# Performance work log

Hardware: AMD Instinct MI355X
Metric: run time of the kernel (lower is better)

The kernel has to match this reference:

```python
import jax, jax.numpy as jnp
import numpy as np

# dims: N batch, I input ch, R recurrent ch, A attention ch, HEADS, O out ch, HxW spatial
N, I, R, A, HEADS, O, H, W = 8, 128, 256, 256, 8, 256, 36, 36
HC = A // HEADS  # head channels


def _conv(x, w, pad):
    # NCHW conv, stride 1
    return jax.lax.conv_general_dilated(x, w, (1, 1), pad,
                                        dimension_numbers=('NCHW', 'OIHW', 'NCHW'))


def setup_inputs() -> dict:
    key = jax.random.key(0)
    ks = jax.random.split(key, 16)

    def wgt(k, shape):
        fan_in = int(np.prod(shape[1:]))
        return jax.random.normal(k, shape, jnp.float32) * (1.0 / float(np.sqrt(fan_in)))

    # gate biases: [init_input=-1 | init_forget=1 | 0 | 0] per CvtLstm init
    b_g = jnp.concatenate([jnp.full((R,), -1.0), jnp.full((R,), 1.0),
                           jnp.zeros((R,)), jnp.zeros((R,))]).astype(jnp.float32)

    return {
        'x': jax.random.normal(ks[0], (N, I, H, W), jnp.float32),
        'w_in': wgt(ks[1], (R, I, 1, 1)), 'b_in': jnp.zeros((R,), jnp.float32),
        'w_qx': wgt(ks[2], (A, R, 3, 3)), 'w_qh': wgt(ks[3], (A, R, 3, 3)),
        'w_kx': wgt(ks[4], (A, R, 3, 3)), 'w_kh': wgt(ks[5], (A, R, 3, 3)),
        'w_vx': wgt(ks[6], (A, R, 3, 3)), 'w_vh': wgt(ks[7], (A, R, 3, 3)),
        'w_ga': wgt(ks[8], (4 * R, A, 1, 1)), 'b_g': b_g,
        'w_gx': wgt(ks[9], (4 * R, R, 1, 1)), 'w_gh': wgt(ks[10], (4 * R, R, 1, 1)),
        'w_out': wgt(ks[11], (O, R, 1, 1)), 'b_out': jnp.zeros((O,), jnp.float32),
    }


def reference(x, w_in, b_in, w_qx, w_qh, w_kx, w_kh, w_vx, w_vh,
              w_ga, b_g, w_gx, w_gh, w_out, b_out):
    # input accumulate: 1x1 conv + bias
    xin = _conv(x, w_in, 'SAME') + b_in[None, :, None, None]
    # first step: recurrent state is zeros (past is empty)
    h = jnp.zeros_like(xin)
    c = jnp.zeros_like(xin)
    # Q: 3x3 padded conv on x and h (accumulated); K/V: 3x3 unpadded -> smaller token set
    q = (_conv(xin, w_qx, 'SAME') + _conv(h, w_qh, 'SAME')).reshape(N, HEADS, HC, H * W)
    k4 = _conv(xin, w_kx, 'VALID') + _conv(h, w_kh, 'VALID')   # [N, A, H-2, W-2]
    D = k4.shape[2] * k4.shape[3]
    k = k4.reshape(N, HEADS, HC, D)
    v = (_conv(xin, w_vx, 'VALID') + _conv(h, w_vh, 'VALID')).reshape(N, HEADS, HC, D)
    # attention: softmax over K/V tokens (dim D)
    attn = jax.nn.softmax(jnp.einsum('nhcq,nhcd->nhqd', q, k), axis=3)  # [N,HEADS,Q,D]
    a = jnp.einsum('nhcd,nhqd->nhcq', v, attn).reshape(N, A, H, W)
    # fused i/f/g/o gate projections: 1x1 conv on a + bias + 1x1 skips on x and h
    gates = (_conv(a, w_ga, 'SAME') + b_g[None, :, None, None]
             + _conv(xin, w_gx, 'SAME') + _conv(h, w_gh, 'SAME'))
    gi, gf, gg, go = jnp.split(gates, 4, axis=1)
    c = jax.nn.sigmoid(gf) * c + jax.nn.sigmoid(gi) * jnp.tanh(gg)
    hn = jax.nn.sigmoid(go) * jnp.tanh(c)
    # output 1x1 conv (dropout p=0 -> identity)
    return _conv(hn, w_out, 'SAME') + b_out[None, :, None, None]
```

## Files before the change

### kernel.cpp

```cpp
#include <hip/hip_runtime.h>
#include <math.h>

typedef unsigned int u32;
typedef unsigned short u16;
typedef unsigned long long u64;
typedef __attribute__((ext_vector_type(8))) __bf16 bf8;
typedef __attribute__((ext_vector_type(4))) float f4;

#define MFMA(a,b,c) __builtin_amdgcn_mfma_f32_16x16x32_bf16(a,b,c,0,0,0)

#define SWC(row_, c_) ((((((c_)>>1) ^ (((row_)>>3)&1))<<1) | (((c_)&1) ^ (((row_)>>4)&1))))

static __device__ __forceinline__ u32 cvtpk(float lo, float hi) {
  u32 r; asm("v_cvt_pk_bf16_f32 %0, %1, %2" : "=v"(r) : "v"(lo), "v"(hi));
  return r;
}
static __device__ __forceinline__ u16 f2b(float x) { return (u16)cvtpk(x, 0.f); }
static __device__ __forceinline__ float sigm(float x) { return 1.f/(1.f+__expf(-x)); }


__global__ __launch_bounds__(256) void k_prep(const float* __restrict__ w_in,
        const float* __restrict__ w_out,
        const float* __restrict__ wqx, const float* __restrict__ wkx,
        const float* __restrict__ wvx,
        const float* __restrict__ w_ga, const float* __restrict__ w_gx,
        u16* __restrict__ winb, u16* __restrict__ woutb,
        u16* __restrict__ tq, u16* __restrict__ tk, u16* __restrict__ tv,
        u16* __restrict__ wg) {
  int task = blockIdx.y;
  int i = blockIdx.x*256 + threadIdx.x;
  if (task == 0) {
    if (i < 32768) winb[i] = f2b(w_in[i]);
    else if (i < 98304) woutb[i - 32768] = f2b(w_out[i - 32768]);
  } else if (task <= 3) {
    if (i < 589824) {
      const float* w = (task==1)?wqx:(task==2)?wkx:wvx;
      u16* wt = (task==1)?tq:(task==2)?tk:tv;
      int e = i & 7, li = (i>>3) & 15, gr = (i>>7) & 3, mb = (i>>9) & 15, it = i >> 13;
      int tap = it >> 3, kg = it & 7;
      int m = mb*16 + li, k = kg*32 + gr*8 + e;
      wt[i] = f2b(w[(size_t)m*2304 + k*9 + tap]);
    }
  } else {
    if (i < 393216) {
      int g = i >> 17, rem = i & 131071, rr = rem >> 9, kk = rem & 511;
      int gb = (g == 0) ? 0 : (g == 1) ? 512 : 768;
      float v = (kk < 256) ? w_ga[(size_t)(gb+rr)*256 + kk]
                           : w_gx[(size_t)(gb+rr)*256 + kk - 256];
      wg[i] = f2b(v);
    }
  }
}

__global__ __launch_bounds__(256,2) void k_xin(const float* __restrict__ x,
        const u16* __restrict__ wb, const float* __restrict__ bias,
        u16* __restrict__ out) {
  __shared__ alignas(16) u16 Xs[128][40];
  __shared__ alignas(16) u16 Ws[128][40];
  int tid = threadIdx.x, lane = tid & 63, wid = tid >> 6;
  int li = lane & 15, gr = lane >> 4;
  int p0 = blockIdx.x*128, m0 = blockIdx.y*128, n = blockIdx.z;
  int pcol = tid & 127, rg = tid >> 7;
  int wrow = tid >> 1, wh = tid & 1;
  int p = p0 + pcol;
  const float* src = x + (size_t)n*128*1296;
  const u32* wb32 = (const u32*)wb;
  f4 z = {0.f,0.f,0.f,0.f};
  f4 acc[4][4];
  #pragma unroll
  for (int i=0;i<4;i++) { acc[i][0]=z; acc[i][1]=z; acc[i][2]=z; acc[i][3]=z; }
  int wm = (wid & 1)*64, wp = (wid >> 1)*64;
  for (int k0 = 0; k0 < 128; k0 += 32) {
    u32 rx[8];
    #pragma unroll
    for (int j = 0; j < 8; j++) {
      int rp = rg*8 + j;
      float a = 0.f, b = 0.f;
      if (p < 1296) { a = src[(size_t)(k0+2*rp)*1296+p]; b = src[(size_t)(k0+2*rp+1)*1296+p]; }
      rx[j] = cvtpk(a, b);
    }
    const u32* wsrc = wb32 + (size_t)(m0+wrow)*64 + (k0>>1) + wh*8;
    int4 rwA = *(const int4*)wsrc, rwB = *(const int4*)(wsrc+4);
    *(int4*)&Xs[pcol][SWC(pcol,2*rg)*8]   = *(int4*)&rx[0];
    *(int4*)&Xs[pcol][SWC(pcol,2*rg+1)*8] = *(int4*)&rx[4];
    *(int4*)&Ws[wrow][SWC(wrow,2*wh)*8]   = rwA;
    *(int4*)&Ws[wrow][SWC(wrow,2*wh+1)*8] = rwB;
    __syncthreads();
    bf8 af[4], bx[4];
    #pragma unroll
    for (int mt=0;mt<4;mt++) { int r = wm+mt*16+li; af[mt] = *(bf8*)&Ws[r][SWC(r,gr)*8]; }
    #pragma unroll
    for (int pt=0;pt<4;pt++) { int r = wp+pt*16+li; bx[pt] = *(bf8*)&Xs[r][SWC(r,gr)*8]; }
    #pragma unroll
    for (int mt=0;mt<4;mt++)
      #pragma unroll
      for (int pt=0;pt<4;pt++)
        acc[mt][pt] = MFMA(af[mt], bx[pt], acc[mt][pt]);
    __syncthreads();
  }
  u32* out32 = (u32*)out + (size_t)n*128*1296;
  #pragma unroll
  for (int mt=0;mt<4;mt++)
    #pragma unroll
    for (int pt=0;pt<4;pt++) {
      int mb = m0 + wm + mt*16 + gr*4;
      int pp = p0 + wp + pt*16 + li;
      if (pp < 1296) {
        out32[(size_t)(mb>>1)*1296 + pp] = cvtpk(acc[mt][pt][0]+bias[mb], acc[mt][pt][1]+bias[mb+1]);
        out32[(size_t)((mb>>1)+1)*1296 + pp] = cvtpk(acc[mt][pt][2]+bias[mb+2], acc[mt][pt][3]+bias[mb+3]);
      }
    }
}

__global__ __launch_bounds__(256,2) void k_conv3(const u16* __restrict__ xin,
        const u16* __restrict__ wq, const u16* __restrict__ wk, const u16* __restrict__ wv,
        u16* __restrict__ qb, u16* __restrict__ kb, u16* __restrict__ vb) {
  __shared__ alignas(16) u16 Xs[2][256][32];
  int tid = threadIdx.x, lane = tid & 63, wid = tid >> 6;
  int li = lane & 15, gr = lane >> 4;
  int tile = blockIdx.x, m0 = blockIdx.y*64, n = blockIdx.z;
  int kind, t0;
  if (tile < 6)       { kind = 0; t0 = tile; }
  else if (tile < 11) { kind = 1; t0 = tile - 6; }
  else                { kind = 2; t0 = tile - 11; }
  int P  = kind ? 1156 : 1296;
  int WO = kind ? 34 : 36;
  int pad = kind ? 0 : 1;
  int px0 = t0*256;
  const u16* wt = (kind==0) ? wq : (kind==1) ? wk : wv;
  const u32* src32 = (const u32*)xin + (size_t)n*128*1296;
  const int4* wt4 = (const int4*)wt;
  int p = px0 + tid;
  bool pvld = p < P;
  int py = 0, px = 0;
  if (pvld) { py = p / WO; px = p % WO; }
  int fx = (tid >> 1) & 3;
  int fr = (li >> 1) & 3;
  int mb0 = m0 >> 4;
  f4 z = {0.f,0.f,0.f,0.f};
  f4 acc[4][4];
  #pragma unroll
  for (int i=0;i<4;i++) { acc[i][0]=z; acc[i][1]=z; acc[i][2]=z; acc[i][3]=z; }
  u32 xA[16], xB[16];
  int4 wA[4], wB[4];

  #define LOADX(it_, X) { \
    int tap_ = (it_) >> 3, kg_ = (it_) & 7; \
    int sy = py + tap_/3 - pad, sx = px + tap_%3 - pad; \
    bool ok = pvld && sy >= 0 && sy < 36 && sx >= 0 && sx < 36; \
    const u32* xs = src32 + (size_t)(kg_*16)*1296 + sy*36 + sx; \
    _Pragma("unroll") \
    for (int j = 0; j < 16; j++) X[j] = ok ? xs[(size_t)j*1296] : 0u; }

  #define LOADW(it_, W) { \
    const int4* wsrc = wt4 + ((size_t)(it_)*16 + mb0)*64 + lane; \
    _Pragma("unroll") \
    for (int mt = 0; mt < 4; mt++) W[mt] = wsrc[(size_t)mt*64]; }

  #define WRITEX(X, b_) { \
    _Pragma("unroll") \
    for (int c = 0; c < 4; c++) \
      *(int4*)&Xs[b_][tid][(c ^ fx)*8] = *(int4*)&X[c*4]; }

  #define MFMAIT(b_, W) { \
    bf8 bx[4]; \
    _Pragma("unroll") \
    for (int pt=0;pt<4;pt++) { \
      int r = wid*64 + pt*16 + li; \
      bx[pt] = *(bf8*)&Xs[b_][r][(gr ^ fr)*8]; \
    } \
    _Pragma("unroll") \
    for (int mt=0;mt<4;mt++) \
      _Pragma("unroll") \
      for (int pt=0;pt<4;pt++) \
        acc[mt][pt] = MFMA(*(bf8*)&W[mt], bx[pt], acc[mt][pt]); }

  LOADX(0, xA); LOADW(0, wA);
  WRITEX(xA, 0);
  LOADX(1, xB); LOADW(1, wB);
  for (int h = 0; h < 35; h++) {
    MFMAIT(0, wA);
    WRITEX(xB, 1);
    LOADX(2*h+2, xA); LOADW(2*h+2, wA);
    MFMAIT(1, wB);
    WRITEX(xA, 0);
    LOADX(2*h+3, xB); LOADW(2*h+3, wB);
  }
  MFMAIT(0, wA);
  WRITEX(xB, 1);
  MFMAIT(1, wB);
  #undef LOADX
  #undef LOADW
  #undef WRITEX
  #undef MFMAIT

  if (kind <= 1) {
    u32* dst32 = (u32*)(kind==0 ? qb : kb) + (size_t)n*128*P;
    #pragma unroll
    for (int mt=0;mt<4;mt++)
      #pragma unroll
      for (int pt=0;pt<4;pt++) {
        int mb = m0 + mt*16 + gr*4;
        int pp = px0 + wid*64 + pt*16 + li;
        if (pp < P) {
          dst32[(size_t)(mb>>1)*P + pp] = cvtpk(acc[mt][pt][0], acc[mt][pt][1]);
          dst32[(size_t)((mb>>1)+1)*P + pp] = cvtpk(acc[mt][pt][2], acc[mt][pt][3]);
        }
      }
  } else {
    #pragma unroll
    for (int mt=0;mt<4;mt++)
      #pragma unroll
      for (int pt=0;pt<4;pt++) {
        int pp = px0 + wid*64 + pt*16 + li;
        if (pp < P) {
          #pragma unroll
          for (int j=0;j<4;j++) {
            int m = m0 + mt*16 + gr*4 + j;
            vb[((size_t)n*256 + m)*1156 + pp] = f2b(acc[mt][pt][j]);
          }
        }
      }
  }
}

__global__ __launch_bounds__(256,2) void k_attn(const u16* __restrict__ qbf,
        const u16* __restrict__ kbf, const u16* __restrict__ vbf, u16* __restrict__ abf) {
  __shared__ alignas(16) u16 Qs[128][40];
  __shared__ alignas(16) u16 Ks[64][40];
  __shared__ alignas(16) u16 Vs[2][32][40];
  __shared__ alignas(16) u16 Ps[4][2][32][40];
  int tid = threadIdx.x, lane = tid & 63, wid = tid >> 6;
  int li = lane & 15, gr = lane >> 4;
  int h = blockIdx.y, n = blockIdx.z;
  int q0 = blockIdx.x*128;
  const u32* Qp32 = (const u32*)qbf + ((size_t)n*128 + h*16)*1296;
  const u32* Kp32 = (const u32*)kbf + ((size_t)n*128 + h*16)*1156;
  const u16* Vp = vbf + ((size_t)n*256 + h*32)*1156;
  #pragma unroll
  for (int j = 0; j < 8; j++) {
    int idx = tid + j*256, qq = idx >> 4, cp = idx & 15;
    int gq = q0 + qq;
    ((u32*)&Qs[qq][0])[cp] = (gq < 1296) ? Qp32[(size_t)cp*1296 + gq] : 0u;
  }
  f4 z = {0.f,0.f,0.f,0.f};
  float mx[2] = {-1e30f, -1e30f}, ls[2] = {0.f, 0.f};
  f4 accO[2][2] = {{z,z},{z,z}};
  int wq = wid*32;
  int kdd = tid >> 2, kq = tid & 3;
  __syncthreads();
  for (int d0 = 0; d0 < 1156; d0 += 64) {
    {
      u32 kk[4];
      int gd = d0 + kdd;
      #pragma unroll
      for (int i = 0; i < 4; i++)
        kk[i] = (gd < 1156) ? Kp32[(size_t)(kq*4+i)*1156 + gd] : 0u;
      *(int4*)&Ks[kdd][SWC(kdd,kq)*8] = *(int4*)&kk[0];
    }
    #pragma unroll
    for (int j = 0; j < 4; j++) {
      int idx = tid + j*256, half = idx >> 9, rem = idx & 511;
      int cc = rem >> 4, dp = rem & 15;
      int gd = d0 + half*32 + dp*2; u32 v = 0;
      if (gd < 1156) v = *(const u32*)&Vp[(size_t)cc*1156 + gd];
      ((u32*)&Vs[half][cc][0])[dp] = v;
    }
    __syncthreads();
    bf8 ak[4], bq[2];
    #pragma unroll
    for (int dt=0;dt<4;dt++) { int r = dt*16+li; ak[dt] = *(bf8*)&Ks[r][SWC(r,gr)*8]; }
    #pragma unroll
    for (int qt=0;qt<2;qt++) bq[qt] = *(bf8*)&Qs[wq + qt*16 + li][8*gr];
    f4 s[2][4];
    #pragma unroll
    for (int qt=0;qt<2;qt++)
      #pragma unroll
      for (int dt=0;dt<4;dt++)
        s[qt][dt] = MFMA(ak[dt], bq[qt], z);
    bool tail = (d0 + 64 > 1156);
    #pragma unroll
    for (int qt=0;qt<2;qt++) {
      if (tail) {
        #pragma unroll
        for (int dt=0;dt<4;dt++)
          #pragma unroll
          for (int j=0;j<4;j++)
            if (d0 + dt*16 + gr*4 + j >= 1156) s[qt][dt][j] = -1e30f;
      }
      float tm = -1e30f;
      #pragma unroll
      for (int dt=0;dt<4;dt++)
        #pragma unroll
        for (int j=0;j<4;j++) tm = fmaxf(tm, s[qt][dt][j]);
      tm = fmaxf(tm, __shfl_xor(tm, 16));
      tm = fmaxf(tm, __shfl_xor(tm, 32));
      if (__any(tm > mx[qt] + 8.f)) {
        float nm = fmaxf(mx[qt], tm);
        float corr = __expf(mx[qt] - nm);
        mx[qt] = nm;
        ls[qt] *= corr;
        accO[0][qt] *= corr; accO[1][qt] *= corr;
      }
      float rs = 0.f;
      #pragma unroll
      for (int dt=0;dt<4;dt++)
        #pragma unroll
        for (int j=0;j<4;j++) {
          float e = __expf(s[qt][dt][j] - mx[qt]);
          s[qt][dt][j] = e; rs += e;
        }
      rs += __shfl_xor(rs, 16); rs += __shfl_xor(rs, 32);
      ls[qt] += rs;
      #pragma unroll
      for (int dt=0;dt<4;dt++) {
        u32 lo_ = cvtpk(s[qt][dt][0], s[qt][dt][1]);
        u32 hi_ = cvtpk(s[qt][dt][2], s[qt][dt][3]);
        u64 pk = (u64)lo_ | ((u64)hi_ << 32);
        *(u64*)&Ps[wid][dt>>1][qt*16 + li][(dt&1)*16 + gr*4] = pk;
      }
    }
    #pragma unroll
    for (int kt=0;kt<2;kt++) {
      bf8 av0 = *(bf8*)&Vs[kt][li][8*gr];
      bf8 av1 = *(bf8*)&Vs[kt][16 + li][8*gr];
      bf8 bp0 = *(bf8*)&Ps[wid][kt][li][8*gr];
      bf8 bp1 = *(bf8*)&Ps[wid][kt][16 + li][8*gr];
      accO[0][0] = MFMA(av0, bp0, accO[0][0]);
      accO[0][1] = MFMA(av0, bp1, accO[0][1]);
      accO[1][0] = MFMA(av1, bp0, accO[1][0]);
      accO[1][1] = MFMA(av1, bp1, accO[1][1]);
    }
    __syncthreads();
  }
  u32* ab32 = (u32*)abf + (size_t)n*128*1296;
  #pragma unroll
  for (int qt=0;qt<2;qt++) {
    float inv = 1.f / ls[qt];
    #pragma unroll
    for (int mt=0;mt<2;mt++) {
      int cb = h*32 + mt*16 + gr*4;
      int gq = q0 + wq + qt*16 + li;
      if (gq < 1296) {
        ab32[(size_t)(cb>>1)*1296 + gq] = cvtpk(accO[mt][qt][0]*inv, accO[mt][qt][1]*inv);
        ab32[(size_t)((cb>>1)+1)*1296 + gq] = cvtpk(accO[mt][qt][2]*inv, accO[mt][qt][3]*inv);
      }
    }
  }
}

__global__ __launch_bounds__(256,2) void k_gates(const u16* __restrict__ abf,
        const u16* __restrict__ xin, const u16* __restrict__ wg,
        const float* __restrict__ b_g, u16* __restrict__ hn) {
  __shared__ alignas(16) u16 Xs[128][40];
  __shared__ alignas(16) u16 Wg[3][64][40];
  int tid = threadIdx.x, lane = tid & 63, wid = tid >> 6;
  int li = lane & 15, gr = lane >> 4;
  int p0 = blockIdx.x*128, m0 = blockIdx.y*64, n = blockIdx.z;
  int pcol = tid & 127, rg = tid >> 7;
  int p = p0 + pcol;
  const u32* wg32 = (const u32*)wg;
  f4 z = {0.f,0.f,0.f,0.f};
  f4 acc[3][2][4];
  #pragma unroll
  for (int g=0;g<3;g++)
    #pragma unroll
    for (int mt=0;mt<2;mt++) { acc[g][mt][0]=z; acc[g][mt][1]=z; acc[g][mt][2]=z; acc[g][mt][3]=z; }
  int wm = (wid & 1)*32, wp = (wid >> 1)*64;
  for (int k0 = 0; k0 < 512; k0 += 32) {
    const u32* src32 = (const u32*)((k0 < 256) ? abf : xin)
        + (size_t)n*128*1296 + (size_t)((k0 & 255)>>1)*1296;
    u32 rx[8];
    #pragma unroll
    for (int j = 0; j < 8; j++) {
      int rp = rg*8 + j;
      rx[j] = (p < 1296) ? src32[(size_t)rp*1296 + p] : 0u;
    }
    *(int4*)&Xs[pcol][SWC(pcol,2*rg)*8]   = *(int4*)&rx[0];
    *(int4*)&Xs[pcol][SWC(pcol,2*rg+1)*8] = *(int4*)&rx[4];
    #pragma unroll
    for (int j = 0; j < 3; j++) {
      int sid = tid + j*256;
      int rid = sid >> 2, q = sid & 3;
      int g = rid >> 6, mm = rid & 63;
      const u32* wsrc = wg32 + (size_t)g*65536 + (size_t)(m0+mm)*256 + (k0>>1) + q*4;
      int4 w4 = *(const int4*)wsrc;
      *(int4*)&Wg[g][mm][SWC(mm,q)*8] = w4;
    }
    __syncthreads();
    bf8 bx[4];
    #pragma unroll
    for (int pt=0;pt<4;pt++) { int r = wp+pt*16+li; bx[pt] = *(bf8*)&Xs[r][SWC(r,gr)*8]; }
    #pragma unroll
    for (int g=0;g<3;g++)
      #pragma unroll
      for (int mt=0;mt<2;mt++) {
        int r = wm+mt*16+li;
        bf8 af = *(bf8*)&Wg[g][r][SWC(r,gr)*8];
        #pragma unroll
        for (int pt=0;pt<4;pt++)
          acc[g][mt][pt] = MFMA(af, bx[pt], acc[g][mt][pt]);
      }
    __syncthreads();
  }
  u32* hn32 = (u32*)hn + (size_t)n*128*1296;
  #pragma unroll
  for (int mt=0;mt<2;mt++)
    #pragma unroll
    for (int pt=0;pt<4;pt++) {
      int rb = m0 + wm + mt*16 + gr*4;
      int pp = p0 + wp + pt*16 + li;
      if (pp < 1296) {
        float hv[4];
        #pragma unroll
        for (int j=0;j<4;j++) {
          float gi = acc[0][mt][pt][j] + b_g[rb+j];
          float gg = acc[1][mt][pt][j] + b_g[512 + rb+j];
          float go = acc[2][mt][pt][j] + b_g[768 + rb+j];
          hv[j] = sigm(go) * tanhf(sigm(gi) * tanhf(gg));
        }
        hn32[(size_t)(rb>>1)*1296 + pp] = cvtpk(hv[0], hv[1]);
        hn32[(size_t)((rb>>1)+1)*1296 + pp] = cvtpk(hv[2], hv[3]);
      }
    }
}

__global__ __launch_bounds__(256,2) void k_out(const u16* __restrict__ hn,
        const u16* __restrict__ wb, const float* __restrict__ bias,
        float* __restrict__ out) {
  __shared__ alignas(16) u16 Xs[128][40];
  __shared__ alignas(16) u16 Ws[128][40];
  int tid = threadIdx.x, lane = tid & 63, wid = tid >> 6;
  int li = lane & 15, gr = lane >> 4;
  int p0 = blockIdx.x*128, m0 = blockIdx.y*128, n = blockIdx.z;
  int pcol = tid & 127, rg = tid >> 7;
  int wrow = tid >> 1, wh = tid & 1;
  int p = p0 + pcol;
  const u32* src32 = (const u32*)hn + (size_t)n*128*1296;
  const u32* wb32 = (const u32*)wb;
  f4 z = {0.f,0.f,0.f,0.f};
  f4 acc[4][4];
  #pragma unroll
  for (int i=0;i<4;i++) { acc[i][0]=z; acc[i][1]=z; acc[i][2]=z; acc[i][3]=z; }
  int wm = (wid & 1)*64, wp = (wid >> 1)*64;
  for (int k0 = 0; k0 < 256; k0 += 32) {
    u32 rx[8];
    #pragma unroll
    for (int j = 0; j < 8; j++) {
      int rp = rg*8 + j;
      rx[j] = (p < 1296) ? src32[(size_t)((k0>>1) + rp)*1296 + p] : 0u;
    }
    const u32* wsrc = wb32 + (size_t)(m0+wrow)*128 + (k0>>1) + wh*8;
    int4 rwA = *(const int4*)wsrc, rwB = *(const int4*)(wsrc+4);
    *(int4*)&Xs[pcol][SWC(pcol,2*rg)*8]   = *(int4*)&rx[0];
    *(int4*)&Xs[pcol][SWC(pcol,2*rg+1)*8] = *(int4*)&rx[4];
    *(int4*)&Ws[wrow][SWC(wrow,2*wh)*8]   = rwA;
    *(int4*)&Ws[wrow][SWC(wrow,2*wh+1)*8] = rwB;
    __syncthreads();
    bf8 af[4], bx[4];
    #pragma unroll
    for (int mt=0;mt<4;mt++) { int r = wm+mt*16+li; af[mt] = *(bf8*)&Ws[r][SWC(r,gr)*8]; }
    #pragma unroll
    for (int pt=0;pt<4;pt++) { int r = wp+pt*16+li; bx[pt] = *(bf8*)&Xs[r][SWC(r,gr)*8]; }
    #pragma unroll
    for (int mt=0;mt<4;mt++)
      #pragma unroll
      for (int pt=0;pt<4;pt++)
        acc[mt][pt] = MFMA(af[mt], bx[pt], acc[mt][pt]);
    __syncthreads();
  }
  #pragma unroll
  for (int mt=0;mt<4;mt++)
    #pragma unroll
    for (int pt=0;pt<4;pt++)
      #pragma unroll
      for (int j=0;j<4;j++) {
        int m = m0 + wm + mt*16 + gr*4 + j;
        int pp = p0 + wp + pt*16 + li;
        if (pp < 1296) out[((size_t)n*256 + m)*1296 + pp] = acc[mt][pt][j] + bias[m];
      }
}

extern "C" void kernel_launch(void* const* d_in, const int* in_sizes, int n_in,
                              void* d_out, int out_size, void* d_ws, size_t ws_size,
                              hipStream_t stream) {
  const float* x     = (const float*)d_in[0];
  const float* w_in  = (const float*)d_in[1];
  const float* b_in  = (const float*)d_in[2];
  const float* w_qx  = (const float*)d_in[3];
  const float* w_kx  = (const float*)d_in[5];
  const float* w_vx  = (const float*)d_in[7];
  const float* w_ga  = (const float*)d_in[9];
  const float* b_g   = (const float*)d_in[10];
  const float* w_gx  = (const float*)d_in[11];
  const float* w_out = (const float*)d_in[13];
  const float* b_out = (const float*)d_in[14];
  float* out = (float*)d_out;

  u16* ws = (u16*)d_ws;
  size_t o = 0;
  u16* xin_bf = ws + o; o += 2654208;
  u16* qbuf   = ws + o; o += 2654208;
  u16* kbuf   = ws + o; o += 2367488;
  u16* vbuf   = ws + o; o += 2367488;
  u16* abuf   = ws + o; o += 2654208;
  u16* hnb    = ws + o; o += 2654208;
  u16* wqT    = ws + o; o += 589824;
  u16* wkT    = ws + o; o += 589824;
  u16* wvT    = ws + o; o += 589824;
  u16* wgT    = ws + o; o += 393216;
  u16* winb   = ws + o; o += 32768;
  u16* woutb  = ws + o; o += 65536;

  k_prep<<<dim3(2304,5), 256, 0, stream>>>(w_in, w_out, w_qx, w_kx, w_vx,
                                           w_ga, w_gx, winb, woutb, wqT, wkT, wvT, wgT);

  k_xin  <<<dim3(11,2,8), 256, 0, stream>>>(x, winb, b_in, xin_bf);
  k_conv3<<<dim3(16,4,8), 256, 0, stream>>>(xin_bf, wqT, wkT, wvT, qbuf, kbuf, vbuf);
  k_attn <<<dim3(11,8,8), 256, 0, stream>>>(qbuf, kbuf, vbuf, abuf);
  k_gates<<<dim3(11,4,8), 256, 0, stream>>>(abuf, xin_bf, wgT, b_g, hnb);
  k_out  <<<dim3(11,2,8), 256, 0, stream>>>(hnb, woutb, b_out, out);
}
```

Before: 201.4 us.

## Stage haloed input tile once per channel group and reuse across nine conv taps

The 3x3 conv kernel now loads a haloed spatial patch (up to 384 positions) of 32 input channels into shared memory once per channel group, then reads all nine taps from it through precomputed swizzled offsets. Previously it reloaded gathered inputs from global memory for every tap. The weight prep is reordered to kg-major/tap-minor so weights stream in the new loop order. This cuts global/L2 gather traffic by roughly the tap count, at the cost of more LDS, more offset registers (36 ints), and a sync per channel group instead of per tap.

```diff
diff --git a/kernel.cpp b/kernel.cpp
--- a/kernel.cpp
+++ b/kernel.cpp
@@ -37,7 +37,7 @@
       const float* w = (task==1)?wqx:(task==2)?wkx:wvx;
       u16* wt = (task==1)?tq:(task==2)?tk:tv;
       int e = i & 7, li = (i>>3) & 15, gr = (i>>7) & 3, mb = (i>>9) & 15, it = i >> 13;
-      int tap = it >> 3, kg = it & 7;
+      int tap = it % 9, kg = it / 9;
       int m = mb*16 + li, k = kg*32 + gr*8 + e;
       wt[i] = f2b(w[(size_t)m*2304 + k*9 + tap]);
     }
@@ -115,7 +115,7 @@
 __global__ __launch_bounds__(256,2) void k_conv3(const u16* __restrict__ xin,
         const u16* __restrict__ wq, const u16* __restrict__ wk, const u16* __restrict__ wv,
         u16* __restrict__ qb, u16* __restrict__ kb, u16* __restrict__ vb) {
-  __shared__ alignas(16) u16 Xs[2][256][32];
+  __shared__ alignas(16) u16 XF[2*384*32];
   int tid = threadIdx.x, lane = tid & 63, wid = tid >> 6;
   int li = lane & 15, gr = lane >> 4;
   int tile = blockIdx.x, m0 = blockIdx.y*64, n = blockIdx.z;
@@ -125,74 +125,111 @@
   else                { kind = 2; t0 = tile - 11; }
   int P  = kind ? 1156 : 1296;
   int WO = kind ? 34 : 36;
-  int pad = kind ? 0 : 1;
   int px0 = t0*256;
   const u16* wt = (kind==0) ? wq : (kind==1) ? wk : wv;
   const u32* src32 = (const u32*)xin + (size_t)n*128*1296;
   const int4* wt4 = (const int4*)wt;
-  int p = px0 + tid;
-  bool pvld = p < P;
-  int py = 0, px = 0;
-  if (pvld) { py = p / WO; px = p % WO; }
-  int fx = (tid >> 1) & 3;
-  int fr = (li >> 1) & 3;
   int mb0 = m0 >> 4;
+
+  int g0, g1; bool v0, v1;
+  if (kind == 0) {
+    int ry0 = px0/36 - 1;
+    int r_ = tid/38, c_ = tid%38;
+    int sy = ry0 + r_, sx = c_ - 1;
+    v0 = (sy >= 0 && sy < 36 && sx >= 0 && sx < 36);
+    g0 = v0 ? sy*36 + sx : 0;
+    int lpx1 = tid + 256;
+    r_ = lpx1/38; c_ = lpx1%38;
+    sy = ry0 + r_; sx = c_ - 1;
+    v1 = (sy >= 0 && sy < 36 && sx >= 0 && sx < 36);
+    g1 = v1 ? sy*36 + sx : 0;
+  } else {
+    int smin = px0 + 2*(px0/34);
+    int s0 = smin + tid, s1 = smin + tid + 256;
+    v0 = s0 < 1296; v1 = s1 < 1296;
+    g0 = v0 ? s0 : 0; g1 = v1 ? s1 : 0;
+  }
+  int sw0 = (tid >> 1) & 3;
+
+  int rdo[4][9];
+  {
+    int rs = kind ? 36 : 38;
+    int py0q = px0/36, smin = px0 + 2*(px0/34);
+    #pragma unroll
+    for (int pt = 0; pt < 4; pt++) {
+      int p = px0 + wid*64 + pt*16 + li;
+      if (p > P-1) p = P-1;
+      int py = p / WO, pxc = p % WO;
+      int lb = kind ? (p + 2*py - smin) : ((py - py0q)*38 + pxc);
+      #pragma unroll
+      for (int tp = 0; tp < 9; tp++) {
+        int lp = lb + (tp/3)*rs + tp%3;
+        rdo[pt][tp] = lp*32 + ((gr ^ ((lp>>1)&3)) << 3);
+      }
+    }
+  }
+
   f4 z = {0.f,0.f,0.f,0.f};
   f4 acc[4][4];
   #pragma unroll
   for (int i=0;i<4;i++) { acc[i][0]=z; acc[i][1]=z; acc[i][2]=z; acc[i][3]=z; }
-  u32 xA[16], xB[16];
-  int4 wA[4], wB[4];
-
-  #define LOADX(it_, X) { \
-    int tap_ = (it_) >> 3, kg_ = (it_) & 7; \
-    int sy = py + tap_/3 - pad, sx = px + tap_%3 - pad; \
-    bool ok = pvld && sy >= 0 && sy < 36 && sx >= 0 && sx < 36; \
-    const u32* xs = src32 + (size_t)(kg_*16)*1296 + sy*36 + sx; \
+  u32 sA[16], sB[16];
+  int4 wbuf[2][4];
+
+  #define STAGELOAD(kg_) { \
+    const u32* s_ = src32 + (size_t)((kg_)*16)*1296; \
     _Pragma("unroll") \
-    for (int j = 0; j < 16; j++) X[j] = ok ? xs[(size_t)j*1296] : 0u; }
-
-  #define LOADW(it_, W) { \
-    const int4* wsrc = wt4 + ((size_t)(it_)*16 + mb0)*64 + lane; \
-    _Pragma("unroll") \
-    for (int mt = 0; mt < 4; mt++) W[mt] = wsrc[(size_t)mt*64]; }
-
-  #define WRITEX(X, b_) { \
+    for (int j = 0; j < 16; j++) sA[j] = v0 ? s_[(size_t)j*1296 + g0] : 0u; \
+    if (tid < 128) { \
+      _Pragma("unroll") \
+      for (int j = 0; j < 16; j++) sB[j] = v1 ? s_[(size_t)j*1296 + g1] : 0u; \
+    } }
+
+  #define WRITESTAGE(bb_) { \
+    u16* pl_ = &XF[(bb_)*12288]; \
     _Pragma("unroll") \
     for (int c = 0; c < 4; c++) \
-      *(int4*)&Xs[b_][tid][(c ^ fx)*8] = *(int4*)&X[c*4]; }
-
-  #define MFMAIT(b_, W) { \
-    bf8 bx[4]; \
+      *(int4*)&pl_[tid*32 + ((c ^ sw0) << 3)] = *(int4*)&sA[c*4]; \
+    if (tid < 128) { \
+      _Pragma("unroll") \
+      for (int c = 0; c < 4; c++) \
+        *(int4*)&pl_[(tid+256)*32 + ((c ^ sw0) << 3)] = *(int4*)&sB[c*4]; \
+    } }
+
+  #define LOADW(it_) { \
+    const int4* ws_ = wt4 + ((size_t)(it_)*16 + mb0)*64 + lane; \
     _Pragma("unroll") \
-    for (int pt=0;pt<4;pt++) { \
-      int r = wid*64 + pt*16 + li; \
-      bx[pt] = *(bf8*)&Xs[b_][r][(gr ^ fr)*8]; \
-    } \
+    for (int mt = 0; mt < 4; mt++) wbuf[(it_)&1][mt] = ws_[(size_t)mt*64]; }
+
+  #define TAP(kg_, tap_) { \
+    if ((kg_)*9 + (tap_) < 71) LOADW((kg_)*9 + (tap_) + 1); \
+    const u16* pl_ = &XF[((kg_)&1)*12288]; \
+    bf8 bx_[4]; \
     _Pragma("unroll") \
-    for (int mt=0;mt<4;mt++) \
+    for (int pt = 0; pt < 4; pt++) bx_[pt] = *(bf8*)&pl_[rdo[pt][tap_]]; \
+    _Pragma("unroll") \
+    for (int mt = 0; mt < 4; mt++) \
       _Pragma("unroll") \
-      for (int pt=0;pt<4;pt++) \
-        acc[mt][pt] = MFMA(*(bf8*)&W[mt], bx[pt], acc[mt][pt]); }
-
-  LOADX(0, xA); LOADW(0, wA);
-  WRITEX(xA, 0);
-  LOADX(1, xB); LOADW(1, wB);
-  for (int h = 0; h < 35; h++) {
-    MFMAIT(0, wA);
-    WRITEX(xB, 1);
-    LOADX(2*h+2, xA); LOADW(2*h+2, wA);
-    MFMAIT(1, wB);
-    WRITEX(xA, 0);
-    LOADX(2*h+3, xB); LOADW(2*h+3, wB);
-  }
-  MFMAIT(0, wA);
-  WRITEX(xB, 1);
-  MFMAIT(1, wB);
-  #undef LOADX
+      for (int pt = 0; pt < 4; pt++) \
+        acc[mt][pt] = MFMA(*(bf8*)&wbuf[((kg_)*9+(tap_))&1][mt], bx_[pt], acc[mt][pt]); }
+
+  #define KGBODY(kg_) { \
+    if ((kg_) < 7) STAGELOAD((kg_)+1); \
+    TAP(kg_,0) TAP(kg_,1) TAP(kg_,2) TAP(kg_,3) TAP(kg_,4) \
+    TAP(kg_,5) TAP(kg_,6) TAP(kg_,7) TAP(kg_,8) \
+    if ((kg_) < 7) { WRITESTAGE(((kg_)+1)&1); __syncthreads(); } }
+
+  STAGELOAD(0);
+  LOADW(0);
+  WRITESTAGE(0);
+  __syncthreads();
+  KGBODY(0) KGBODY(1) KGBODY(2) KGBODY(3)
+  KGBODY(4) KGBODY(5) KGBODY(6) KGBODY(7)
+  #undef STAGELOAD
+  #undef WRITESTAGE
   #undef LOADW
-  #undef WRITEX
-  #undef MFMAIT
+  #undef TAP
+  #undef KGBODY
 
   if (kind <= 1) {
     u32* dst32 = (u32*)(kind==0 ? qb : kb) + (size_t)n*128*P;
```

Measured after the change: 200.1 us. About the same (-0.7%).
